# Kernel tuning notes

Measured on AMD Instinct MI355X. Metric: run time of the kernel, lower is better.

## Reference

```python
import jax, jax.numpy as jnp
import numpy as np

EPS = 1e-8

def setup_inputs() -> dict:
    key = jax.random.key(0)
    k1, k2 = jax.random.split(key)
    B, C, T_text, max_len = 16, 256, 512, 4096
    x = jax.random.normal(k1, (B, C, T_text), dtype=jnp.float32)
    # positive linear-domain durations, mean ~ max_len / T_text = 8
    w = jax.random.uniform(k2, (B, T_text), dtype=jnp.float32) * 16.0
    x_mask = jnp.ones((B, 1, T_text), dtype=jnp.float32)
    y_mask = jnp.ones((B, 1, max_len), dtype=jnp.float32)
    sigma_scale = jnp.ones((1,), dtype=jnp.float32)
    return {"x": x, "w": w, "x_mask": x_mask, "y_mask": y_mask, "sigma_scale": sigma_scale}

def reference(x, w, x_mask, y_mask, sigma_scale):
    # x: (B, C, T_text), w: (B, T_text), y_mask: (B, 1, max_len)
    x = x * x_mask
    center = jnp.cumsum(w, axis=1) - 0.5 * w            # (B, T_text)
    max_len = y_mask.shape[2]
    pos = jnp.arange(max_len, dtype=x.dtype)            # (max_len,)
    mu = pos[None, None, :] - center[:, :, None]        # (B, T_text, max_len)
    sigma = w[:, :, None] * sigma_scale[0]              # (B, T_text, 1)
    weights = jnp.exp(-0.5 * jnp.square(mu) / (jnp.square(sigma) + EPS))
    weights = weights / (jnp.sum(weights, axis=1, keepdims=True) + EPS)
    upsampled = jnp.einsum('bct,btl->bcl', x, weights)  # (B, C, max_len)
    return upsampled * y_mask
```

## Files before the change

kernel.cpp:

```cpp
#include <hip/hip_runtime.h>
#include <hip/hip_bf16.h>

#define EPS 1e-8f

#define BB 16
#define CC 256
#define TT 512
#define LL 4096
#define KC  32
#define TCB 128
#define TLB 128
#define XR  40

typedef __attribute__((ext_vector_type(8))) short short8;
typedef __attribute__((ext_vector_type(4))) float f32x4;

__device__ __forceinline__ unsigned short bfbits(float f) {
    __hip_bfloat16 h = __float2bfloat16(f);
    return *(unsigned short*)&h;
}
__device__ __forceinline__ unsigned int pack2(float lo, float hi) {
    return (unsigned int)bfbits(lo) | ((unsigned int)bfbits(hi) << 16);
}


#define EXPW(tc_, buf_)                                                         \
    {                                                                           \
        _Pragma("unroll")                                                       \
        for (int i_ = 0; i_ < 2; ++i_) {                                        \
            const int slot  = tid + 256 * i_;                                   \
            const int l_loc = slot >> 2;                                        \
            const int tg    = slot & 3;                                         \
            const int t0    = (tc_) + tg * 8;                                   \
            const float4 cv0 = *(const float4*)&cen_s[t0];                      \
            const float4 cv1 = *(const float4*)&cen_s[t0 + 4];                  \
            const float4 nv0 = *(const float4*)&nh_s[t0];                       \
            const float4 nv1 = *(const float4*)&nh_s[t0 + 4];                   \
            const float4 xk0 = *(const float4*)&xm_s[t0];                       \
            const float4 xk1 = *(const float4*)&xm_s[t0 + 4];                   \
            const float posf = (float)(l0 + l_loc);                             \
            float mu, e0, e1, e2, e3, e4, e5, e6, e7;                           \
            mu = posf - cv0.x; e0 = __expf(mu * mu * nv0.x);                    \
            mu = posf - cv0.y; e1 = __expf(mu * mu * nv0.y);                    \
            mu = posf - cv0.z; e2 = __expf(mu * mu * nv0.z);                    \
            mu = posf - cv0.w; e3 = __expf(mu * mu * nv0.w);                    \
            mu = posf - cv1.x; e4 = __expf(mu * mu * nv1.x);                    \
            mu = posf - cv1.y; e5 = __expf(mu * mu * nv1.y);                    \
            mu = posf - cv1.z; e6 = __expf(mu * mu * nv1.z);                    \
            mu = posf - cv1.w; e7 = __expf(mu * mu * nv1.w);                    \
            const float ps = ((e0 + e1) + (e2 + e3)) + ((e4 + e5) + (e6 + e7)); \
            if (i_ == 0) p0 += ps; else p1 += ps;                               \
            uint4 pk;                                                           \
            pk.x = pack2(e0 * xk0.x, e1 * xk0.y);                               \
            pk.y = pack2(e2 * xk0.z, e3 * xk0.w);                               \
            pk.z = pack2(e4 * xk1.x, e5 * xk1.y);                               \
            pk.w = pack2(e6 * xk1.z, e7 * xk1.w);                               \
            *(uint4*)&ws[buf_][l_loc][tg * 8] = pk;                             \
        }                                                                       \
    }

#define AFRAG(AF, crow_, tc_)                                                   \
    {                                                                           \
        const float* xp = &x[xbase + (size_t)(crow_) * TT + (tc_) + lg * 8];    \
        const float4 a0 = *(const float4*)xp;                                   \
        const float4 a1 = *(const float4*)(xp + 4);                             \
        uint4 ap;                                                               \
        ap.x = pack2(a0.x, a0.y);                                               \
        ap.y = pack2(a0.z, a0.w);                                               \
        ap.z = pack2(a1.x, a1.y);                                               \
        ap.w = pack2(a1.z, a1.w);                                               \
        AF = *(short8*)&ap;                                                     \
    }

#define MFMA_STEP(buf_, tc_)                                                    \
    {                                                                           \
        short8 af0, af1;                                                        \
        AFRAG(af0, wv * 32 + lq, tc_);                                          \
        AFRAG(af1, wv * 32 + 16 + lq, tc_);                                     \
        _Pragma("unroll")                                                       \
        for (int n = 0; n < 8; ++n) {                                           \
            const short8 bfr = *(const short8*)&ws[buf_][n * 16 + lq][lg * 8];  \
            acc0[n] = __builtin_amdgcn_mfma_f32_16x16x32_bf16(af0, bfr, acc0[n], 0, 0, 0); \
            acc1[n] = __builtin_amdgcn_mfma_f32_16x16x32_bf16(af1, bfr, acc1[n], 0, 0, 0); \
        }                                                                       \
    }

__global__ __launch_bounds__(256, 4)
void fused_kernel(const float* __restrict__ x,
                  const float* __restrict__ w,
                  const float* __restrict__ x_mask,
                  const float* __restrict__ y_mask,
                  const float* __restrict__ sigma_scale,
                  float* __restrict__ out) {
    __shared__ unsigned short ws[2][TLB][XR];
    __shared__ float cen_s[TT], nh_s[TT], xm_s[TT];
    __shared__ float dsum[TLB], sscale[TLB];
    __shared__ float part[4], wmx[4], offs[4];
    __shared__ float sdelta;
    __shared__ int tmin_s, tmax_s;

    const int gid = blockIdx.x;
    const int lid = (gid & 7) * 128 + (gid >> 3);
    const int b   = lid >> 6;
    const int rr  = lid & 63;
    const int l0  = (rr >> 1) * TLB;
    const int c0  = (rr & 1) * TCB;

    const int tid  = threadIdx.x;
    const int lane = tid & 63;
    const int wid  = tid >> 6;
    const int wv   = wid;
    const int lq   = lane & 15;
    const int lg   = lane >> 4;
    const int bTT  = b * TT;
    const size_t xbase = (size_t)(b * CC + c0) * TT;

    if (tid == 0) { tmin_s = TT; tmax_s = -1; }

    const int t2 = tid * 2;
    const float2 w2  = *(const float2*)&w[bTT + t2];
    const float2 xm2 = *(const float2*)&x_mask[bTT + t2];
    const float ss = sigma_scale[0];
    const float pairsum = w2.x + w2.y;
    float v = pairsum;
#pragma unroll
    for (int o = 1; o < 64; o <<= 1) {
        float u = __shfl_up(v, o);
        if (lane >= o) v += u;
    }
    float pm = fmaxf(w2.x, w2.y);
#pragma unroll
    for (int o = 1; o < 64; o <<= 1) pm = fmaxf(pm, __shfl_xor(pm, o));
    if (lane == 63) part[wid] = v;
    if (lane == 0)  wmx[wid] = pm;
    __syncthreads();
    if (tid == 0) {
        float run = 0.0f, mm = 0.0f;
#pragma unroll
        for (int i = 0; i < 4; ++i) {
            offs[i] = run;
            run += part[i];
            mm = fmaxf(mm, wmx[i]);
        }
        sdelta = 8.0f * (mm * ss + 1e-4f) + 1.0f;
    }
    __syncthreads();
    const float base = offs[wid] + v - pairsum;
    const float cum1 = base + w2.x;
    const float cum2 = cum1 + w2.y;
    const float cenA = cum1 - 0.5f * w2.x;
    const float cenB = cum2 - 0.5f * w2.y;
    cen_s[t2]     = cenA;
    cen_s[t2 + 1] = cenB;
    const float sgA = w2.x * ss, sgB = w2.y * ss;
    nh_s[t2]     = -0.5f / (sgA * sgA + EPS);
    nh_s[t2 + 1] = -0.5f / (sgB * sgB + EPS);
    xm_s[t2]     = xm2.x;
    xm_s[t2 + 1] = xm2.y;

    const float D  = sdelta;
    const float lo = (float)l0 - D;
    const float hi = (float)(l0 + TLB - 1) + D;
    if (cenA >= lo && cenA <= hi) { atomicMin(&tmin_s, t2);     atomicMax(&tmax_s, t2); }
    if (cenB >= lo && cenB <= hi) { atomicMin(&tmin_s, t2 + 1); atomicMax(&tmax_s, t2 + 1); }
    __syncthreads();
    const int tlo = tmin_s & ~(KC - 1);
    const int nch = (tmax_s >= 0) ? ((((tmax_s & ~(KC - 1)) + KC) - tlo) / KC) : 0;

    f32x4 acc0[8], acc1[8];
#pragma unroll
    for (int n = 0; n < 8; ++n) { acc0[n] = (f32x4)0.0f; acc1[n] = (f32x4)0.0f; }
    float p0 = 0.0f, p1 = 0.0f;

    if (nch > 0) {
        EXPW(tlo, 0);
        __syncthreads();
        for (int i = 0; i < nch; ++i) {
            const int cur = i & 1;
            if (i + 1 < nch) EXPW(tlo + (i + 1) * KC, cur ^ 1);
            MFMA_STEP(cur, tlo + i * KC);
            __syncthreads();
        }
    }

    p0 += __shfl_xor(p0, 1); p0 += __shfl_xor(p0, 2);
    p1 += __shfl_xor(p1, 1); p1 += __shfl_xor(p1, 2);
    if ((tid & 3) == 0) {
        dsum[tid >> 2]        = p0;
        dsum[(tid >> 2) + 64] = p1;
    }
    __syncthreads();
    if (tid < TLB)
        sscale[tid] = y_mask[b * LL + l0 + tid] / (dsum[tid] + EPS);
    __syncthreads();

    float sc[8];
#pragma unroll
    for (int n = 0; n < 8; ++n) sc[n] = sscale[n * 16 + lq];

    const size_t obase = (size_t)(b * CC + c0) * LL + l0;
#pragma unroll
    for (int r = 0; r < 4; ++r) {
        const int cA = wv * 32 + lg * 4 + r;
        float* opA = &out[obase + (size_t)cA * LL];
#pragma unroll
        for (int n = 0; n < 8; ++n) opA[n * 16 + lq] = acc0[n][r] * sc[n];
        float* opB = opA + 16 * LL;
#pragma unroll
        for (int n = 0; n < 8; ++n) opB[n * 16 + lq] = acc1[n][r] * sc[n];
    }
}

extern "C" void kernel_launch(void* const* d_in, const int* in_sizes, int n_in,
                              void* d_out, int out_size, void* d_ws, size_t ws_size,
                              hipStream_t stream) {
    const float* x           = (const float*)d_in[0];
    const float* w           = (const float*)d_in[1];
    const float* x_mask      = (const float*)d_in[2];
    const float* y_mask      = (const float*)d_in[3];
    const float* sigma_scale = (const float*)d_in[4];
    float* out = (float*)d_out;

    hipLaunchKernelGGL(fused_kernel, dim3((LL / TLB) * (CC / TCB) * BB), dim3(256), 0, stream,
                       x, w, x_mask, y_mask, sigma_scale, out);
}
```

Baseline: 24.29 us.

## Halve output tile length and use per-token sigma window for chunk pruning

Shrinks the output time tile from 128 to 64 positions, which doubles the grid and halves per-block MFMA accumulators, Gaussian work and output writes. The range of text tokens is now chosen per token with an 8-sigma window, replacing the global maximum-width window, so fewer K-chunks are visited per block. The cost is that each block stages more x fragments relative to its useful output, since every 64-column tile reloads the same channel rows, and x traffic from L2 grows.

```diff
diff --git a/kernel.cpp b/kernel.cpp
--- a/kernel.cpp
+++ b/kernel.cpp
@@ -9,7 +9,7 @@
 #define LL 4096
 #define KC  32
 #define TCB 128
-#define TLB 128
+#define TLB 64
 #define XR  40
 
 typedef __attribute__((ext_vector_type(8))) short short8;
@@ -26,37 +26,32 @@
 
 #define EXPW(tc_, buf_)                                                         \
     {                                                                           \
-        _Pragma("unroll")                                                       \
-        for (int i_ = 0; i_ < 2; ++i_) {                                        \
-            const int slot  = tid + 256 * i_;                                   \
-            const int l_loc = slot >> 2;                                        \
-            const int tg    = slot & 3;                                         \
-            const int t0    = (tc_) + tg * 8;                                   \
-            const float4 cv0 = *(const float4*)&cen_s[t0];                      \
-            const float4 cv1 = *(const float4*)&cen_s[t0 + 4];                  \
-            const float4 nv0 = *(const float4*)&nh_s[t0];                       \
-            const float4 nv1 = *(const float4*)&nh_s[t0 + 4];                   \
-            const float4 xk0 = *(const float4*)&xm_s[t0];                       \
-            const float4 xk1 = *(const float4*)&xm_s[t0 + 4];                   \
-            const float posf = (float)(l0 + l_loc);                             \
-            float mu, e0, e1, e2, e3, e4, e5, e6, e7;                           \
-            mu = posf - cv0.x; e0 = __expf(mu * mu * nv0.x);                    \
-            mu = posf - cv0.y; e1 = __expf(mu * mu * nv0.y);                    \
-            mu = posf - cv0.z; e2 = __expf(mu * mu * nv0.z);                    \
-            mu = posf - cv0.w; e3 = __expf(mu * mu * nv0.w);                    \
-            mu = posf - cv1.x; e4 = __expf(mu * mu * nv1.x);                    \
-            mu = posf - cv1.y; e5 = __expf(mu * mu * nv1.y);                    \
-            mu = posf - cv1.z; e6 = __expf(mu * mu * nv1.z);                    \
-            mu = posf - cv1.w; e7 = __expf(mu * mu * nv1.w);                    \
-            const float ps = ((e0 + e1) + (e2 + e3)) + ((e4 + e5) + (e6 + e7)); \
-            if (i_ == 0) p0 += ps; else p1 += ps;                               \
-            uint4 pk;                                                           \
-            pk.x = pack2(e0 * xk0.x, e1 * xk0.y);                               \
-            pk.y = pack2(e2 * xk0.z, e3 * xk0.w);                               \
-            pk.z = pack2(e4 * xk1.x, e5 * xk1.y);                               \
-            pk.w = pack2(e6 * xk1.z, e7 * xk1.w);                               \
-            *(uint4*)&ws[buf_][l_loc][tg * 8] = pk;                             \
-        }                                                                       \
+        const int l_loc = tid >> 2;                                             \
+        const int tg    = tid & 3;                                              \
+        const int t0    = (tc_) + tg * 8;                                       \
+        const float4 cv0 = *(const float4*)&cen_s[t0];                          \
+        const float4 cv1 = *(const float4*)&cen_s[t0 + 4];                      \
+        const float4 nv0 = *(const float4*)&nh_s[t0];                           \
+        const float4 nv1 = *(const float4*)&nh_s[t0 + 4];                       \
+        const float4 xk0 = *(const float4*)&xm_s[t0];                           \
+        const float4 xk1 = *(const float4*)&xm_s[t0 + 4];                       \
+        const float posf = (float)(l0 + l_loc);                                 \
+        float mu, e0, e1, e2, e3, e4, e5, e6, e7;                               \
+        mu = posf - cv0.x; e0 = __expf(mu * mu * nv0.x);                        \
+        mu = posf - cv0.y; e1 = __expf(mu * mu * nv0.y);                        \
+        mu = posf - cv0.z; e2 = __expf(mu * mu * nv0.z);                        \
+        mu = posf - cv0.w; e3 = __expf(mu * mu * nv0.w);                        \
+        mu = posf - cv1.x; e4 = __expf(mu * mu * nv1.x);                        \
+        mu = posf - cv1.y; e5 = __expf(mu * mu * nv1.y);                        \
+        mu = posf - cv1.z; e6 = __expf(mu * mu * nv1.z);                        \
+        mu = posf - cv1.w; e7 = __expf(mu * mu * nv1.w);                        \
+        p0 += ((e0 + e1) + (e2 + e3)) + ((e4 + e5) + (e6 + e7));                \
+        uint4 pk;                                                               \
+        pk.x = pack2(e0 * xk0.x, e1 * xk0.y);                                   \
+        pk.y = pack2(e2 * xk0.z, e3 * xk0.w);                                   \
+        pk.z = pack2(e4 * xk1.x, e5 * xk1.y);                                   \
+        pk.w = pack2(e6 * xk1.z, e7 * xk1.w);                                   \
+        *(uint4*)&ws[buf_][l_loc][tg * 8] = pk;                                 \
     }
 
 #define AFRAG(AF, crow_, tc_)                                                   \
@@ -78,7 +73,7 @@
         AFRAG(af0, wv * 32 + lq, tc_);                                          \
         AFRAG(af1, wv * 32 + 16 + lq, tc_);                                     \
         _Pragma("unroll")                                                       \
-        for (int n = 0; n < 8; ++n) {                                           \
+        for (int n = 0; n < 4; ++n) {                                           \
             const short8 bfr = *(const short8*)&ws[buf_][n * 16 + lq][lg * 8];  \
             acc0[n] = __builtin_amdgcn_mfma_f32_16x16x32_bf16(af0, bfr, acc0[n], 0, 0, 0); \
             acc1[n] = __builtin_amdgcn_mfma_f32_16x16x32_bf16(af1, bfr, acc1[n], 0, 0, 0); \
@@ -95,14 +90,13 @@
     __shared__ unsigned short ws[2][TLB][XR];
     __shared__ float cen_s[TT], nh_s[TT], xm_s[TT];
     __shared__ float dsum[TLB], sscale[TLB];
-    __shared__ float part[4], wmx[4], offs[4];
-    __shared__ float sdelta;
+    __shared__ float part[4], offs[4];
     __shared__ int tmin_s, tmax_s;
 
     const int gid = blockIdx.x;
-    const int lid = (gid & 7) * 128 + (gid >> 3);
-    const int b   = lid >> 6;
-    const int rr  = lid & 63;
+    const int lid = (gid & 7) * 256 + (gid >> 3);
+    const int b   = lid >> 7;
+    const int rr  = lid & 127;
     const int l0  = (rr >> 1) * TLB;
     const int c0  = (rr & 1) * TCB;
 
@@ -128,21 +122,12 @@
         float u = __shfl_up(v, o);
         if (lane >= o) v += u;
     }
-    float pm = fmaxf(w2.x, w2.y);
-#pragma unroll
-    for (int o = 1; o < 64; o <<= 1) pm = fmaxf(pm, __shfl_xor(pm, o));
     if (lane == 63) part[wid] = v;
-    if (lane == 0)  wmx[wid] = pm;
     __syncthreads();
     if (tid == 0) {
-        float run = 0.0f, mm = 0.0f;
-#pragma unroll
-        for (int i = 0; i < 4; ++i) {
-            offs[i] = run;
-            run += part[i];
-            mm = fmaxf(mm, wmx[i]);
-        }
-        sdelta = 8.0f * (mm * ss + 1e-4f) + 1.0f;
+        float run = 0.0f;
+#pragma unroll
+        for (int i = 0; i < 4; ++i) { offs[i] = run; run += part[i]; }
     }
     __syncthreads();
     const float base = offs[wid] + v - pairsum;
@@ -158,19 +143,24 @@
     xm_s[t2]     = xm2.x;
     xm_s[t2 + 1] = xm2.y;
 
-    const float D  = sdelta;
-    const float lo = (float)l0 - D;
-    const float hi = (float)(l0 + TLB - 1) + D;
-    if (cenA >= lo && cenA <= hi) { atomicMin(&tmin_s, t2);     atomicMax(&tmax_s, t2); }
-    if (cenB >= lo && cenB <= hi) { atomicMin(&tmin_s, t2 + 1); atomicMax(&tmax_s, t2 + 1); }
+    const float l0f = (float)l0;
+    const float l1f = l0f + (float)(TLB - 1);
+    const float rA = 8.0f * sgA + 1.0f;
+    const float rB = 8.0f * sgB + 1.0f;
+    if (cenA + rA >= l0f && cenA - rA <= l1f) {
+        atomicMin(&tmin_s, t2); atomicMax(&tmax_s, t2);
+    }
+    if (cenB + rB >= l0f && cenB - rB <= l1f) {
+        atomicMin(&tmin_s, t2 + 1); atomicMax(&tmax_s, t2 + 1);
+    }
     __syncthreads();
     const int tlo = tmin_s & ~(KC - 1);
     const int nch = (tmax_s >= 0) ? ((((tmax_s & ~(KC - 1)) + KC) - tlo) / KC) : 0;
 
-    f32x4 acc0[8], acc1[8];
-#pragma unroll
-    for (int n = 0; n < 8; ++n) { acc0[n] = (f32x4)0.0f; acc1[n] = (f32x4)0.0f; }
-    float p0 = 0.0f, p1 = 0.0f;
+    f32x4 acc0[4], acc1[4];
+#pragma unroll
+    for (int n = 0; n < 4; ++n) { acc0[n] = (f32x4)0.0f; acc1[n] = (f32x4)0.0f; }
+    float p0 = 0.0f;
 
     if (nch > 0) {
         EXPW(tlo, 0);
@@ -184,19 +174,15 @@
     }
 
     p0 += __shfl_xor(p0, 1); p0 += __shfl_xor(p0, 2);
-    p1 += __shfl_xor(p1, 1); p1 += __shfl_xor(p1, 2);
-    if ((tid & 3) == 0) {
-        dsum[tid >> 2]        = p0;
-        dsum[(tid >> 2) + 64] = p1;
-    }
+    if ((tid & 3) == 0) dsum[tid >> 2] = p0;
     __syncthreads();
     if (tid < TLB)
         sscale[tid] = y_mask[b * LL + l0 + tid] / (dsum[tid] + EPS);
     __syncthreads();
 
-    float sc[8];
-#pragma unroll
-    for (int n = 0; n < 8; ++n) sc[n] = sscale[n * 16 + lq];
+    float sc[4];
+#pragma unroll
+    for (int n = 0; n < 4; ++n) sc[n] = sscale[n * 16 + lq];
 
     const size_t obase = (size_t)(b * CC + c0) * LL + l0;
 #pragma unroll
@@ -204,10 +190,10 @@
         const int cA = wv * 32 + lg * 4 + r;
         float* opA = &out[obase + (size_t)cA * LL];
 #pragma unroll
-        for (int n = 0; n < 8; ++n) opA[n * 16 + lq] = acc0[n][r] * sc[n];
+        for (int n = 0; n < 4; ++n) opA[n * 16 + lq] = acc0[n][r] * sc[n];
         float* opB = opA + 16 * LL;
 #pragma unroll
-        for (int n = 0; n < 8; ++n) opB[n * 16 + lq] = acc1[n][r] * sc[n];
+        for (int n = 0; n < 4; ++n) opB[n * 16 + lq] = acc1[n][r] * sc[n];
     }
 }
 
```

After: 25.08 us. 1.03x slower.
